# Kernel tuning notes

Hardware: AMD Instinct MI355X
Metric: run time of the kernel (lower is better)

The kernel has to match this reference:

```python
import jax, jax.numpy as jnp
import numpy as np

N, E, DIN, H, C, OUT = 50000, 400000, 128, 4, 64, 40
HC = H * C
NEG_SLOPE = 0.2
EPS = 1e-5


def setup_inputs() -> dict:
    keys = iter(jax.random.split(jax.random.key(0), 64))
    def rn(shape, s=1.0):
        return jax.random.normal(next(keys), shape, jnp.float32) * s
    w = 0.05  # small init scale keeps activations stable through 3 layers
    inp = {}
    inp["x"] = rn((N, DIN))
    inp["src"] = jax.random.randint(next(keys), (E,), 0, N, jnp.int32)
    inp["dst"] = jax.random.randint(next(keys), (E,), 0, N, jnp.int32)
    # conv0: 128 -> (H=4, C=64), concat -> 256
    inp["Wl0"] = rn((DIN, HC), w); inp["bl0"] = jnp.zeros((HC,), jnp.float32)
    inp["Wr0"] = rn((DIN, HC), w); inp["br0"] = jnp.zeros((HC,), jnp.float32)
    inp["att0"] = rn((H, C), w);   inp["bc0"] = jnp.zeros((HC,), jnp.float32)
    inp["Ws0"] = rn((DIN, HC), w); inp["bs0"] = jnp.zeros((HC,), jnp.float32)
    inp["g0"] = jnp.ones((HC,), jnp.float32); inp["be0"] = jnp.zeros((HC,), jnp.float32)
    # conv1: 256 -> (4, 64), concat -> 256
    inp["Wl1"] = rn((HC, HC), w); inp["bl1"] = jnp.zeros((HC,), jnp.float32)
    inp["Wr1"] = rn((HC, HC), w); inp["br1"] = jnp.zeros((HC,), jnp.float32)
    inp["att1"] = rn((H, C), w);  inp["bc1"] = jnp.zeros((HC,), jnp.float32)
    inp["Ws1"] = rn((HC, HC), w); inp["bs1"] = jnp.zeros((HC,), jnp.float32)
    inp["g1"] = jnp.ones((HC,), jnp.float32); inp["be1"] = jnp.zeros((HC,), jnp.float32)
    # conv2: 256 -> (4, 40), mean over heads -> 40
    inp["Wl2"] = rn((HC, H * OUT), w); inp["bl2"] = jnp.zeros((H * OUT,), jnp.float32)
    inp["Wr2"] = rn((HC, H * OUT), w); inp["br2"] = jnp.zeros((H * OUT,), jnp.float32)
    inp["att2"] = rn((H, OUT), w);     inp["bc2"] = jnp.zeros((OUT,), jnp.float32)
    inp["Ws2"] = rn((HC, OUT), w);     inp["bs2"] = jnp.zeros((OUT,), jnp.float32)
    return inp


def _gatv2_conv(x, s, d, Wl, bl, Wr, br, att, bc, concat):
    # PyG GATv2Conv: lin_l on source, lin_r on target; e = LeakyReLU(xl_j + xr_i);
    # logit = <e, att>; softmax over edges sharing the same target; msg = xl_j.
    n = x.shape[0]
    h, c = att.shape
    xl = (x @ Wl + bl).reshape(n, h, c)
    xr = (x @ Wr + br).reshape(n, h, c)
    e = jax.nn.leaky_relu(xl[s] + xr[d], NEG_SLOPE)           # [E, H, C]
    logit = jnp.einsum("ehc,hc->eh", e, att)                  # [E, H]
    m = jax.ops.segment_max(logit, d, num_segments=n)          # per-target max
    a = jnp.exp(logit - m[d])
    z = jax.ops.segment_sum(a, d, num_segments=n)
    alpha = a / z[d]                                           # segment softmax
    out = jax.ops.segment_sum(alpha[:, :, None] * xl[s], d, num_segments=n)  # [N,H,C]
    out = out.reshape(n, h * c) if concat else out.mean(axis=1)
    return out + bc


def _bn(x, g, b):
    mu = x.mean(axis=0)
    var = x.var(axis=0)
    return g * (x - mu) / jnp.sqrt(var + EPS) + b


def reference(x, src, dst,
              Wl0, bl0, Wr0, br0, att0, bc0, Ws0, bs0, g0, be0,
              Wl1, bl1, Wr1, br1, att1, bc1, Ws1, bs1, g1, be1,
              Wl2, bl2, Wr2, br2, att2, bc2, Ws2, bs2):
    n = x.shape[0]
    loops = jnp.arange(n, dtype=src.dtype)  # add_self_loops=True (PyG default)
    s = jnp.concatenate([src, loops])
    d = jnp.concatenate([dst, loops])
    x1 = _gatv2_conv(x, s, d, Wl0, bl0, Wr0, br0, att0, bc0, True) + (x @ Ws0 + bs0)
    x1 = jax.nn.relu(_bn(x1, g0, be0))
    h = _gatv2_conv(x1, s, d, Wl1, bl1, Wr1, br1, att1, bc1, True) + (x1 @ Ws1 + bs1)
    x2 = jax.nn.relu(_bn(h, g1, be1))
    out = _gatv2_conv(x2, s, d, Wl2, bl2, Wr2, br2, att2, bc2, False) + (x2 @ Ws2 + bs2)
    return (h, out)
```

## Files before the change

### kernel.cpp

```cpp
#include <hip/hip_runtime.h>
#include <hip/hip_bf16.h>
#include <cstdint>
#include <cstddef>

#define DIN 128
#define HC 256
#define OUTC 40
#define HOUT 160
#define NEG 0.2f
#define BNEPS 1e-5f

typedef float f32x4 __attribute__((ext_vector_type(4)));
typedef __bf16 bf16x8 __attribute__((ext_vector_type(8)));

struct __align__(8) bh4 { __hip_bfloat16 x, y, z, w; };

__device__ __forceinline__ float4 ld4(const float* p) { return *(const float4*)p; }

__device__ __forceinline__ float4 ldb4(const __hip_bfloat16* p) {
    bh4 v = *(const bh4*)p;
    return make_float4(__bfloat162float(v.x), __bfloat162float(v.y),
                       __bfloat162float(v.z), __bfloat162float(v.w));
}

__device__ __forceinline__ void load_lds16(const void* g, void* l) {
    __builtin_amdgcn_global_load_lds((const __attribute__((address_space(1))) void*)g,
                                     (__attribute__((address_space(3))) void*)l, 16, 0, 0);
}

__global__ __launch_bounds__(256)
void gemm_mfma(const __hip_bfloat16* __restrict__ A, const __hip_bfloat16* __restrict__ Wt,
               const float* __restrict__ biasc, __hip_bfloat16* __restrict__ Y,
               int M, int K, int Npad, int gx, int q, int r) {
    __shared__ __hip_bfloat16 smem[128 * 136];
    __hip_bfloat16* As = smem;
    __hip_bfloat16* Bs = smem + 128 * 32;
    const int tid = threadIdx.x;
    const int lane = tid & 63, wid = tid >> 6;
    const int wm = wid >> 1, wn = wid & 1;

    const int orig = blockIdx.x;
    const int xcd = orig & 7, pos = orig >> 3;
    const int wgid = (xcd < r ? xcd * (q + 1) : r * (q + 1) + (xcd - r) * q) + pos;
    const int bn = (wgid % gx) * 128, bm = (wgid / gx) * 128;

    const int srow = lane >> 2;
    const int sseg = (lane & 3) * 8;
    f32x4 acc[4][4] = {};

    for (int k0 = 0; k0 < K; k0 += 32) {
#pragma unroll
        for (int i = 0; i < 2; ++i) {
            int c = 2 * wid + i;
            int ar = bm + 16 * c + srow; if (ar >= M) ar = M - 1;
            load_lds16(A + (size_t)ar * K + k0 + sseg, (char*)As + c * 1024);
            int br = bn + 16 * c + srow;
            load_lds16(Wt + (size_t)br * K + k0 + sseg, (char*)Bs + c * 1024);
        }
        __syncthreads();
        const int rkb = (lane >> 4) * 8;
        bf16x8 af[4], bfr[4];
#pragma unroll
        for (int i = 0; i < 4; ++i) {
            af[i]  = *(const bf16x8*)(As + (wm * 64 + i * 16 + (lane & 15)) * 32 + rkb);
            bfr[i] = *(const bf16x8*)(Bs + (wn * 64 + i * 16 + (lane & 15)) * 32 + rkb);
        }
#pragma unroll
        for (int mi = 0; mi < 4; ++mi)
#pragma unroll
            for (int ni = 0; ni < 4; ++ni)
                acc[mi][ni] = __builtin_amdgcn_mfma_f32_16x16x32_bf16(af[mi], bfr[ni], acc[mi][ni], 0, 0, 0);
        __syncthreads();
    }
    const int cl = lane & 15, rg4 = (lane >> 4) * 4;
#pragma unroll
    for (int ni = 0; ni < 4; ++ni) {
        float bv = biasc[bn + wn * 64 + ni * 16 + cl];
#pragma unroll
        for (int mi = 0; mi < 4; ++mi)
#pragma unroll
            for (int rr = 0; rr < 4; ++rr)
                smem[(wm * 64 + mi * 16 + rg4 + rr) * 136 + wn * 64 + ni * 16 + cl] =
                    __float2bfloat16(acc[mi][ni][rr] + bv);
    }
    __syncthreads();
#pragma unroll
    for (int it = 0; it < 8; ++it) {
        int row = it * 16 + (tid >> 4);
        int gm = bm + row;
        if (gm < M) {
            float4 v = *(const float4*)((const char*)(smem + row * 136) + (tid & 15) * 16);
            *(float4*)(Y + (size_t)gm * Npad + bn + (tid & 15) * 8) = v;
        }
    }
}

__global__ void prep_w_kernel(const float* __restrict__ W0, const float* __restrict__ b0, int n0,
                              const float* __restrict__ W1, const float* __restrict__ b1, int n1,
                              const float* __restrict__ W2, const float* __restrict__ b2, int n2,
                              int K, int Npad, __hip_bfloat16* __restrict__ Wt,
                              float* __restrict__ bc) {
    int idx = blockIdx.x * 256 + threadIdx.x;
    if (idx >= Npad * K) return;
    int n = idx / K, k = idx % K;
    float v = 0.f, bb = 0.f;
    if (n < n0)                { v = W0[(size_t)k * n0 + n];             bb = b0[n]; }
    else if (n < n0 + n1)      { v = W1[(size_t)k * n1 + (n - n0)];      bb = b1[n - n0]; }
    else if (n < n0 + n1 + n2) { v = W2[(size_t)k * n2 + (n - n0 - n1)]; bb = b2[n - n0 - n1]; }
    Wt[(size_t)n * K + k] = __float2bfloat16(v);
    if (k == 0) bc[n] = bb;
}

__global__ void f2b_kernel(const float* __restrict__ X, __hip_bfloat16* __restrict__ Y, int n4) {
    int i = blockIdx.x * 256 + threadIdx.x;
    if (i >= n4) return;
    float4 v = ((const float4*)X)[i];
    bh4 o;
    o.x = __float2bfloat16(v.x); o.y = __float2bfloat16(v.y);
    o.z = __float2bfloat16(v.z); o.w = __float2bfloat16(v.w);
    ((bh4*)Y)[i] = o;
}

__global__ void hist_kernel(const int* __restrict__ dst, int* __restrict__ deg, int E) {
    int e = blockIdx.x * 256 + threadIdx.x;
    if (e < E) atomicAdd(&deg[dst[e]], 1);
}

__global__ __launch_bounds__(256)
void scan1_kernel(int* __restrict__ a, int* __restrict__ bsum, int n) {
    const int tid = threadIdx.x;
    const int i = blockIdx.x * 256 + tid;
    const int lane = tid & 63, w = tid >> 6;
    int v = (i < n) ? (a[i] + 1) : 0;
    int x = v;
#pragma unroll
    for (int s = 1; s < 64; s <<= 1) { int t = __shfl_up(x, s); if (lane >= s) x += t; }
    __shared__ int ws[4];
    if (lane == 63) ws[w] = x;
    __syncthreads();
    int bo = 0;
    if (w > 0) bo = ws[0];
    if (w > 1) bo += ws[1];
    if (w > 2) bo += ws[2];
    if (i <= n) a[i] = bo + x - v;
    if (tid == 255) bsum[blockIdx.x] = bo + x;
}

__global__ __launch_bounds__(256)
void scan2_kernel(int* __restrict__ bsum, int nb) {
    const int tid = threadIdx.x;
    const int lane = tid & 63, w = tid >> 6;
    int v = (tid < nb) ? bsum[tid] : 0;
    int x = v;
#pragma unroll
    for (int s = 1; s < 64; s <<= 1) { int t = __shfl_up(x, s); if (lane >= s) x += t; }
    __shared__ int ws[4];
    if (lane == 63) ws[w] = x;
    __syncthreads();
    int bo = 0;
    if (w > 0) bo = ws[0];
    if (w > 1) bo += ws[1];
    if (w > 2) bo += ws[2];
    if (tid < nb) bsum[tid] = bo + x - v;
}

__global__ void scan3_kernel(int* __restrict__ a, const int* __restrict__ bsum, int n) {
    int i = blockIdx.x * 256 + threadIdx.x;
    if (i <= n) a[i] += bsum[blockIdx.x];
}

__global__ void scatter_kernel(const int* __restrict__ src, const int* __restrict__ dst,
                               const int* __restrict__ off, int* __restrict__ cursor,
                               int* __restrict__ srcs, int E, int N) {
    int e = blockIdx.x * 256 + threadIdx.x;
    if (e >= E + N) return;
    int s, d;
    if (e < E) { s = src[e]; d = dst[e]; }
    else       { s = e - E;  d = e - E; }
    int p = atomicAdd(&cursor[d], 1);
    srcs[off[d] + p] = s;
}

__device__ __forceinline__ float edge_logit(const float4& xl, const float4& xr, const float4& av) {
    float ex = xl.x + xr.x; ex = ex > 0.f ? ex : NEG * ex;
    float ey = xl.y + xr.y; ey = ey > 0.f ? ey : NEG * ey;
    float ez = xl.z + xr.z; ez = ez > 0.f ? ez : NEG * ez;
    float ew = xl.w + xr.w; ew = ew > 0.f ? ew : NEG * ew;
    float p = ex * av.x + ey * av.y + ez * av.z + ew * av.w;
    p += __shfl_xor(p, 1);
    p += __shfl_xor(p, 2);
    p += __shfl_xor(p, 4);
    p += __shfl_xor(p, 8);
    return p;
}

__device__ __forceinline__ void ons_update(float p, const float4& xl, float& m, float& z,
                                           float& ax, float& ay, float& az, float& aw) {
    float mn = fmaxf(m, p);
    float sc = __expf(m - mn);
    float a  = __expf(p - mn);
    m = mn;
    z  = z  * sc + a;
    ax = ax * sc + a * xl.x;
    ay = ay * sc + a * xl.y;
    az = az * sc + a * xl.z;
    aw = aw * sc + a * xl.w;
}

__global__ __launch_bounds__(256)
void gat_conv_cat(const __hip_bfloat16* __restrict__ XL, const __hip_bfloat16* __restrict__ XR,
                  const __hip_bfloat16* __restrict__ SK, const float* __restrict__ att,
                  const float* __restrict__ bc,
                  const int* __restrict__ off, const int* __restrict__ srcs,
                  float* __restrict__ OUT, int N, int RS) {
    int n = blockIdx.x * 4 + (threadIdx.x >> 6);
    if (n >= N) return;
    int lane = threadIdx.x & 63;
    int c4 = lane << 2;
    const float4 xr = ldb4(XR + (size_t)n * RS + c4);
    const float4 av = ld4(att + c4);
    float m = -1e30f, z = 0.f;
    float ax = 0.f, ay = 0.f, az = 0.f, aw = 0.f;
    int j = off[n];
    const int e1 = off[n + 1];
    for (; j + 3 < e1; j += 4) {
        int s0 = srcs[j], s1 = srcs[j + 1], s2 = srcs[j + 2], s3 = srcs[j + 3];
        float4 xl0 = ldb4(XL + (size_t)s0 * RS + c4);
        float4 xl1 = ldb4(XL + (size_t)s1 * RS + c4);
        float4 xl2 = ldb4(XL + (size_t)s2 * RS + c4);
        float4 xl3 = ldb4(XL + (size_t)s3 * RS + c4);
        float p0 = edge_logit(xl0, xr, av);
        float p1 = edge_logit(xl1, xr, av);
        float p2 = edge_logit(xl2, xr, av);
        float p3 = edge_logit(xl3, xr, av);
        ons_update(p0, xl0, m, z, ax, ay, az, aw);
        ons_update(p1, xl1, m, z, ax, ay, az, aw);
        ons_update(p2, xl2, m, z, ax, ay, az, aw);
        ons_update(p3, xl3, m, z, ax, ay, az, aw);
    }
    for (; j < e1; ++j) {
        int s0 = srcs[j];
        float4 xl0 = ldb4(XL + (size_t)s0 * RS + c4);
        float p0 = edge_logit(xl0, xr, av);
        ons_update(p0, xl0, m, z, ax, ay, az, aw);
    }
    float inv = 1.f / z;
    float4 sk = ldb4(SK + (size_t)n * RS + c4);
    float4 bb = ld4(bc + c4);
    float4 r;
    r.x = ax * inv + bb.x + sk.x;
    r.y = ay * inv + bb.y + sk.y;
    r.z = az * inv + bb.z + sk.z;
    r.w = aw * inv + bb.w + sk.w;
    *(float4*)(OUT + (size_t)n * HC + c4) = r;
}

__global__ __launch_bounds__(256)
void gat_conv_mean(const __hip_bfloat16* __restrict__ XL, const __hip_bfloat16* __restrict__ XR,
                   const __hip_bfloat16* __restrict__ SK, const float* __restrict__ att,
                   const float* __restrict__ bc,
                   const int* __restrict__ off, const int* __restrict__ srcs,
                   float* __restrict__ OUT, int N, int RS) {
    int n = blockIdx.x * 4 + (threadIdx.x >> 6);
    if (n >= N) return;
    int lane = threadIdx.x & 63;
    int hd = lane >> 4, q = lane & 15;
    bool act = (q < 10);
    int base = hd * OUTC + (q << 2);
    float4 xr = make_float4(0.f, 0.f, 0.f, 0.f), av = xr;
    if (act) { xr = ldb4(XR + (size_t)n * RS + base); av = ld4(att + base); }
    float m = -1e30f, z = 0.f;
    float ax = 0.f, ay = 0.f, az = 0.f, aw = 0.f;
    int j = off[n];
    const int e1 = off[n + 1];
    const float4 zero = make_float4(0.f, 0.f, 0.f, 0.f);
    for (; j + 3 < e1; j += 4) {
        int s0 = srcs[j], s1 = srcs[j + 1], s2 = srcs[j + 2], s3 = srcs[j + 3];
        float4 xl0 = zero, xl1 = zero, xl2 = zero, xl3 = zero;
        if (act) {
            xl0 = ldb4(XL + (size_t)s0 * RS + base);
            xl1 = ldb4(XL + (size_t)s1 * RS + base);
            xl2 = ldb4(XL + (size_t)s2 * RS + base);
            xl3 = ldb4(XL + (size_t)s3 * RS + base);
        }
        float p0 = edge_logit(xl0, xr, av);
        float p1 = edge_logit(xl1, xr, av);
        float p2 = edge_logit(xl2, xr, av);
        float p3 = edge_logit(xl3, xr, av);
        ons_update(p0, xl0, m, z, ax, ay, az, aw);
        ons_update(p1, xl1, m, z, ax, ay, az, aw);
        ons_update(p2, xl2, m, z, ax, ay, az, aw);
        ons_update(p3, xl3, m, z, ax, ay, az, aw);
    }
    for (; j < e1; ++j) {
        int s0 = srcs[j];
        float4 xl0 = zero;
        if (act) xl0 = ldb4(XL + (size_t)s0 * RS + base);
        float p0 = edge_logit(xl0, xr, av);
        ons_update(p0, xl0, m, z, ax, ay, az, aw);
    }
    float inv = 1.f / z;
    float rx = ax * inv, ry = ay * inv, rz = az * inv, rw = aw * inv;
    rx += __shfl_xor(rx, 16); rx += __shfl_xor(rx, 32);
    ry += __shfl_xor(ry, 16); ry += __shfl_xor(ry, 32);
    rz += __shfl_xor(rz, 16); rz += __shfl_xor(rz, 32);
    rw += __shfl_xor(rw, 16); rw += __shfl_xor(rw, 32);
    if (lane < 10) {
        int o = q << 2;
        float4 sk = ldb4(SK + (size_t)n * RS + o);
        float4 r;
        r.x = rx * 0.25f + bc[o + 0] + sk.x;
        r.y = ry * 0.25f + bc[o + 1] + sk.y;
        r.z = rz * 0.25f + bc[o + 2] + sk.z;
        r.w = rw * 0.25f + bc[o + 3] + sk.w;
        *(float4*)(OUT + (size_t)n * OUTC + o) = r;
    }
}

__global__ __launch_bounds__(256)
void bn_stats_kernel(const float* __restrict__ X, float* __restrict__ sums,
                     float* __restrict__ sqs, int N) {
    int c = threadIdx.x;
    float s = 0.f, qq = 0.f;
    for (int n = blockIdx.x; n < N; n += gridDim.x) {
        float v = X[(size_t)n * HC + c];
        s += v; qq += v * v;
    }
    atomicAdd(&sums[c], s);
    atomicAdd(&sqs[c], qq);
}

__global__ __launch_bounds__(256)
void bn_finalize_kernel(const float* __restrict__ sums, const float* __restrict__ sqs,
                        const float* __restrict__ g, const float* __restrict__ be,
                        float* __restrict__ scale, float* __restrict__ shift, int N) {
    int c = threadIdx.x;
    float mean = sums[c] / (float)N;
    float var = sqs[c] / (float)N - mean * mean;
    float inv = rsqrtf(var + BNEPS);
    float sc = g[c] * inv;
    scale[c] = sc;
    shift[c] = be[c] - mean * sc;
}

__global__ __launch_bounds__(256)
void bn_apply_relu_kernel(const float* __restrict__ X, const float* __restrict__ sc,
                          const float* __restrict__ sh, __hip_bfloat16* __restrict__ Y, int n4) {
    for (int i = blockIdx.x * blockDim.x + threadIdx.x; i < n4; i += gridDim.x * blockDim.x) {
        int c4 = (i & 63) << 2;
        float4 v = ((const float4*)X)[i];
        float4 s = ld4(sc + c4);
        float4 h = ld4(sh + c4);
        bh4 r;
        r.x = __float2bfloat16(fmaxf(v.x * s.x + h.x, 0.f));
        r.y = __float2bfloat16(fmaxf(v.y * s.y + h.y, 0.f));
        r.z = __float2bfloat16(fmaxf(v.z * s.z + h.z, 0.f));
        r.w = __float2bfloat16(fmaxf(v.w * s.w + h.w, 0.f));
        ((bh4*)Y)[i] = r;
    }
}

extern "C" void kernel_launch(void* const* d_in, const int* in_sizes, int n_in,
                              void* d_out, int out_size, void* d_ws, size_t ws_size,
                              hipStream_t stream) {
    const int N = in_sizes[0] / DIN;
    const int E = in_sizes[1];
    const int Et = E + N;

    const float* x   = (const float*)d_in[0];
    const int* src   = (const int*)d_in[1];
    const int* dst   = (const int*)d_in[2];
    const float* Wl0 = (const float*)d_in[3];  const float* bl0 = (const float*)d_in[4];
    const float* Wr0 = (const float*)d_in[5];  const float* br0 = (const float*)d_in[6];
    const float* att0= (const float*)d_in[7];  const float* bc0 = (const float*)d_in[8];
    const float* Ws0 = (const float*)d_in[9];  const float* bs0 = (const float*)d_in[10];
    const float* g0  = (const float*)d_in[11]; const float* be0 = (const float*)d_in[12];
    const float* Wl1 = (const float*)d_in[13]; const float* bl1 = (const float*)d_in[14];
    const float* Wr1 = (const float*)d_in[15]; const float* br1 = (const float*)d_in[16];
    const float* att1= (const float*)d_in[17]; const float* bc1 = (const float*)d_in[18];
    const float* Ws1 = (const float*)d_in[19]; const float* bs1 = (const float*)d_in[20];
    const float* g1  = (const float*)d_in[21]; const float* be1 = (const float*)d_in[22];
    const float* Wl2 = (const float*)d_in[23]; const float* bl2 = (const float*)d_in[24];
    const float* Wr2 = (const float*)d_in[25]; const float* br2 = (const float*)d_in[26];
    const float* att2= (const float*)d_in[27]; const float* bc2 = (const float*)d_in[28];
    const float* Ws2 = (const float*)d_in[29]; const float* bs2 = (const float*)d_in[30];

    float* outh = (float*)d_out;
    float* outy = outh + (size_t)N * HC;

    __hip_bfloat16* Y  = (__hip_bfloat16*)d_ws;
    __hip_bfloat16* xb = Y + (size_t)N * 768;
    __hip_bfloat16* Wt = xb + (size_t)N * HC;
    float* bcc  = (float*)(Wt + 768 * 256);
    int* off    = (int*)(bcc + 768);
    int* cursor = off + (N + 1);
    int* srcs   = cursor + N;
    int* bsum   = srcs + Et;
    float* bn   = (float*)((((uintptr_t)(bsum + 256)) + 15) & ~(uintptr_t)15);

    const int nb_scan = (N + 1 + 255) / 256;
    hipMemsetAsync(off, 0, (size_t)(N + 1) * sizeof(int), stream);
    hipMemsetAsync(cursor, 0, (size_t)N * sizeof(int), stream);
    hist_kernel<<<(E + 255) / 256, 256, 0, stream>>>(dst, off, E);
    scan1_kernel<<<nb_scan, 256, 0, stream>>>(off, bsum, N);
    scan2_kernel<<<1, 256, 0, stream>>>(bsum, nb_scan);
    scan3_kernel<<<nb_scan, 256, 0, stream>>>(off, bsum, N);
    scatter_kernel<<<(Et + 255) / 256, 256, 0, stream>>>(src, dst, off, cursor, srcs, E, N);

    const int gmy = (N + 127) / 128;
    const int convGrid = (N + 3) / 4;
    const int nwgA = 6 * gmy, qA = nwgA / 8, rA = nwgA % 8;
    const int nwgC = 3 * gmy, qC = nwgC / 8, rC = nwgC % 8;

    f2b_kernel<<<(N * DIN / 4 + 255) / 256, 256, 0, stream>>>(x, xb, N * DIN / 4);
    prep_w_kernel<<<(768 * DIN + 255) / 256, 256, 0, stream>>>(
        Wl0, bl0, HC, Wr0, br0, HC, Ws0, bs0, HC, DIN, 768, Wt, bcc);
    gemm_mfma<<<nwgA, 256, 0, stream>>>(xb, Wt, bcc, Y, N, DIN, 768, 6, qA, rA);
    gat_conv_cat<<<convGrid, 256, 0, stream>>>(Y, Y + 256, Y + 512, att0, bc0, off, srcs,
                                               outh, N, 768);
    hipMemsetAsync(bn, 0, 512 * sizeof(float), stream);
    bn_stats_kernel<<<1024, 256, 0, stream>>>(outh, bn, bn + 256, N);
    bn_finalize_kernel<<<1, 256, 0, stream>>>(bn, bn + 256, g0, be0, bn + 512, bn + 768, N);
    bn_apply_relu_kernel<<<2048, 256, 0, stream>>>(outh, bn + 512, bn + 768, xb, N * (HC / 4));

    prep_w_kernel<<<(768 * HC + 255) / 256, 256, 0, stream>>>(
        Wl1, bl1, HC, Wr1, br1, HC, Ws1, bs1, HC, HC, 768, Wt, bcc);
    gemm_mfma<<<nwgA, 256, 0, stream>>>(xb, Wt, bcc, Y, N, HC, 768, 6, qA, rA);
    gat_conv_cat<<<convGrid, 256, 0, stream>>>(Y, Y + 256, Y + 512, att1, bc1, off, srcs,
                                               outh, N, 768);
    hipMemsetAsync(bn, 0, 512 * sizeof(float), stream);
    bn_stats_kernel<<<1024, 256, 0, stream>>>(outh, bn, bn + 256, N);
    bn_finalize_kernel<<<1, 256, 0, stream>>>(bn, bn + 256, g1, be1, bn + 512, bn + 768, N);
    bn_apply_relu_kernel<<<2048, 256, 0, stream>>>(outh, bn + 512, bn + 768, xb, N * (HC / 4));

    prep_w_kernel<<<(384 * HC + 255) / 256, 256, 0, stream>>>(
        Wl2, bl2, HOUT, Wr2, br2, HOUT, Ws2, bs2, OUTC, HC, 384, Wt, bcc);
    gemm_mfma<<<nwgC, 256, 0, stream>>>(xb, Wt, bcc, Y, N, HC, 384, 3, qC, rC);
    gat_conv_mean<<<convGrid, 256, 0, stream>>>(Y, Y + 160, Y + 320, att2, bc2, off, srcs,
                                                outy, N, 384);
}
```

Measured before the change: 448.9 us.

## Drop online-softmax max tracking and repack mean conv to half-wave per node

Replaces the online softmax, which rescales the running max on every edge, with a plain exp-sum accumulation. Logits are clamped at 50 to avoid overflow, so each edge no longer pays the extra exp and rescale multiplies. The head-mean conv now assigns 32 lanes per node (two nodes per wave), with each lane holding 5 channels (a float4 plus one scalar), so no lanes sit idle. The risk is reduced numerical robustness: large negative logits could underflow, and clamping changes results once logits exceed 50.

```diff
diff --git a/kernel.cpp b/kernel.cpp
--- a/kernel.cpp
+++ b/kernel.cpp
@@ -191,20 +191,7 @@
     p += __shfl_xor(p, 2);
     p += __shfl_xor(p, 4);
     p += __shfl_xor(p, 8);
-    return p;
-}
-
-__device__ __forceinline__ void ons_update(float p, const float4& xl, float& m, float& z,
-                                           float& ax, float& ay, float& az, float& aw) {
-    float mn = fmaxf(m, p);
-    float sc = __expf(m - mn);
-    float a  = __expf(p - mn);
-    m = mn;
-    z  = z  * sc + a;
-    ax = ax * sc + a * xl.x;
-    ay = ay * sc + a * xl.y;
-    az = az * sc + a * xl.z;
-    aw = aw * sc + a * xl.w;
+    return fminf(p, 50.f);
 }
 
 __global__ __launch_bounds__(256)
@@ -219,7 +206,7 @@
     int c4 = lane << 2;
     const float4 xr = ldb4(XR + (size_t)n * RS + c4);
     const float4 av = ld4(att + c4);
-    float m = -1e30f, z = 0.f;
+    float z = 0.f;
     float ax = 0.f, ay = 0.f, az = 0.f, aw = 0.f;
     int j = off[n];
     const int e1 = off[n + 1];
@@ -229,20 +216,20 @@
         float4 xl1 = ldb4(XL + (size_t)s1 * RS + c4);
         float4 xl2 = ldb4(XL + (size_t)s2 * RS + c4);
         float4 xl3 = ldb4(XL + (size_t)s3 * RS + c4);
-        float p0 = edge_logit(xl0, xr, av);
-        float p1 = edge_logit(xl1, xr, av);
-        float p2 = edge_logit(xl2, xr, av);
-        float p3 = edge_logit(xl3, xr, av);
-        ons_update(p0, xl0, m, z, ax, ay, az, aw);
-        ons_update(p1, xl1, m, z, ax, ay, az, aw);
-        ons_update(p2, xl2, m, z, ax, ay, az, aw);
-        ons_update(p3, xl3, m, z, ax, ay, az, aw);
+        float a0 = __expf(edge_logit(xl0, xr, av));
+        float a1 = __expf(edge_logit(xl1, xr, av));
+        float a2 = __expf(edge_logit(xl2, xr, av));
+        float a3 = __expf(edge_logit(xl3, xr, av));
+        z += a0; ax += a0 * xl0.x; ay += a0 * xl0.y; az += a0 * xl0.z; aw += a0 * xl0.w;
+        z += a1; ax += a1 * xl1.x; ay += a1 * xl1.y; az += a1 * xl1.z; aw += a1 * xl1.w;
+        z += a2; ax += a2 * xl2.x; ay += a2 * xl2.y; az += a2 * xl2.z; aw += a2 * xl2.w;
+        z += a3; ax += a3 * xl3.x; ay += a3 * xl3.y; az += a3 * xl3.z; aw += a3 * xl3.w;
     }
     for (; j < e1; ++j) {
         int s0 = srcs[j];
         float4 xl0 = ldb4(XL + (size_t)s0 * RS + c4);
-        float p0 = edge_logit(xl0, xr, av);
-        ons_update(p0, xl0, m, z, ax, ay, az, aw);
+        float a0 = __expf(edge_logit(xl0, xr, av));
+        z += a0; ax += a0 * xl0.x; ay += a0 * xl0.y; az += a0 * xl0.z; aw += a0 * xl0.w;
     }
     float inv = 1.f / z;
     float4 sk = ldb4(SK + (size_t)n * RS + c4);
@@ -255,65 +242,79 @@
     *(float4*)(OUT + (size_t)n * HC + c4) = r;
 }
 
+__device__ __forceinline__ void mean_edge(const __hip_bfloat16* __restrict__ XL, size_t srow,
+                                          int bm_ch, int bt_ch,
+                                          const float4& xr4, float xrt,
+                                          const float4& av4, float avt,
+                                          float& z, float& c0, float& c1, float& c2,
+                                          float& c3, float& c4) {
+    float4 x4 = ldb4(XL + srow + bm_ch);
+    float xt = __bfloat162float(XL[srow + bt_ch]);
+    float e0 = x4.x + xr4.x; e0 = e0 > 0.f ? e0 : NEG * e0;
+    float e1 = x4.y + xr4.y; e1 = e1 > 0.f ? e1 : NEG * e1;
+    float e2 = x4.z + xr4.z; e2 = e2 > 0.f ? e2 : NEG * e2;
+    float e3 = x4.w + xr4.w; e3 = e3 > 0.f ? e3 : NEG * e3;
+    float et = xt + xrt;     et = et > 0.f ? et : NEG * et;
+    float p = e0 * av4.x + e1 * av4.y + e2 * av4.z + e3 * av4.w + et * avt;
+    p += __shfl_xor(p, 1);
+    p += __shfl_xor(p, 2);
+    p += __shfl_xor(p, 4);
+    p = fminf(p, 50.f);
+    float a = __expf(p);
+    z += a;
+    c0 += a * x4.x; c1 += a * x4.y; c2 += a * x4.z; c3 += a * x4.w; c4 += a * xt;
+}
+
 __global__ __launch_bounds__(256)
 void gat_conv_mean(const __hip_bfloat16* __restrict__ XL, const __hip_bfloat16* __restrict__ XR,
                    const __hip_bfloat16* __restrict__ SK, const float* __restrict__ att,
                    const float* __restrict__ bc,
                    const int* __restrict__ off, const int* __restrict__ srcs,
                    float* __restrict__ OUT, int N, int RS) {
-    int n = blockIdx.x * 4 + (threadIdx.x >> 6);
+    const int lane = threadIdx.x & 63;
+    const int half = lane >> 5, sub = lane & 31;
+    const int n = blockIdx.x * 8 + (threadIdx.x >> 6) * 2 + half;
     if (n >= N) return;
-    int lane = threadIdx.x & 63;
-    int hd = lane >> 4, q = lane & 15;
-    bool act = (q < 10);
-    int base = hd * OUTC + (q << 2);
-    float4 xr = make_float4(0.f, 0.f, 0.f, 0.f), av = xr;
-    if (act) { xr = ldb4(XR + (size_t)n * RS + base); av = ld4(att + base); }
-    float m = -1e30f, z = 0.f;
-    float ax = 0.f, ay = 0.f, az = 0.f, aw = 0.f;
+    const int hd = sub >> 3, q = sub & 7;
+    const int bm_ch = hd * OUTC + q * 4;
+    const int bt_ch = hd * OUTC + 32 + q;
+    const size_t nrow = (size_t)n * RS;
+    const float4 xr4 = ldb4(XR + nrow + bm_ch);
+    const float xrt = __bfloat162float(XR[nrow + bt_ch]);
+    const float4 av4 = ld4(att + bm_ch);
+    const float avt = att[bt_ch];
+    float z = 0.f, c0 = 0.f, c1 = 0.f, c2 = 0.f, c3 = 0.f, c4 = 0.f;
     int j = off[n];
     const int e1 = off[n + 1];
-    const float4 zero = make_float4(0.f, 0.f, 0.f, 0.f);
     for (; j + 3 < e1; j += 4) {
-        int s0 = srcs[j], s1 = srcs[j + 1], s2 = srcs[j + 2], s3 = srcs[j + 3];
-        float4 xl0 = zero, xl1 = zero, xl2 = zero, xl3 = zero;
-        if (act) {
-            xl0 = ldb4(XL + (size_t)s0 * RS + base);
-            xl1 = ldb4(XL + (size_t)s1 * RS + base);
-            xl2 = ldb4(XL + (size_t)s2 * RS + base);
-            xl3 = ldb4(XL + (size_t)s3 * RS + base);
-        }
-        float p0 = edge_logit(xl0, xr, av);
-        float p1 = edge_logit(xl1, xr, av);
-        float p2 = edge_logit(xl2, xr, av);
-        float p3 = edge_logit(xl3, xr, av);
-        ons_update(p0, xl0, m, z, ax, ay, az, aw);
-        ons_update(p1, xl1, m, z, ax, ay, az, aw);
-        ons_update(p2, xl2, m, z, ax, ay, az, aw);
-        ons_update(p3, xl3, m, z, ax, ay, az, aw);
-    }
-    for (; j < e1; ++j) {
-        int s0 = srcs[j];
-        float4 xl0 = zero;
-        if (act) xl0 = ldb4(XL + (size_t)s0 * RS + base);
-        float p0 = edge_logit(xl0, xr, av);
-        ons_update(p0, xl0, m, z, ax, ay, az, aw);
-    }
+        size_t r0 = (size_t)srcs[j] * RS,     r1 = (size_t)srcs[j + 1] * RS;
+        size_t r2 = (size_t)srcs[j + 2] * RS, r3 = (size_t)srcs[j + 3] * RS;
+        mean_edge(XL, r0, bm_ch, bt_ch, xr4, xrt, av4, avt, z, c0, c1, c2, c3, c4);
+        mean_edge(XL, r1, bm_ch, bt_ch, xr4, xrt, av4, avt, z, c0, c1, c2, c3, c4);
+        mean_edge(XL, r2, bm_ch, bt_ch, xr4, xrt, av4, avt, z, c0, c1, c2, c3, c4);
+        mean_edge(XL, r3, bm_ch, bt_ch, xr4, xrt, av4, avt, z, c0, c1, c2, c3, c4);
+    }
+    for (; j < e1; ++j)
+        mean_edge(XL, (size_t)srcs[j] * RS, bm_ch, bt_ch, xr4, xrt, av4, avt, z, c0, c1, c2, c3, c4);
+
     float inv = 1.f / z;
-    float rx = ax * inv, ry = ay * inv, rz = az * inv, rw = aw * inv;
-    rx += __shfl_xor(rx, 16); rx += __shfl_xor(rx, 32);
-    ry += __shfl_xor(ry, 16); ry += __shfl_xor(ry, 32);
-    rz += __shfl_xor(rz, 16); rz += __shfl_xor(rz, 32);
-    rw += __shfl_xor(rw, 16); rw += __shfl_xor(rw, 32);
-    if (lane < 10) {
+    float r0 = c0 * inv, r1 = c1 * inv, r2 = c2 * inv, r3 = c3 * inv, r4 = c4 * inv;
+    r0 += __shfl_xor(r0, 8); r0 += __shfl_xor(r0, 16);
+    r1 += __shfl_xor(r1, 8); r1 += __shfl_xor(r1, 16);
+    r2 += __shfl_xor(r2, 8); r2 += __shfl_xor(r2, 16);
+    r3 += __shfl_xor(r3, 8); r3 += __shfl_xor(r3, 16);
+    r4 += __shfl_xor(r4, 8); r4 += __shfl_xor(r4, 16);
+    if (hd == 0) {
         int o = q << 2;
-        float4 sk = ldb4(SK + (size_t)n * RS + o);
-        float4 r;
-        r.x = rx * 0.25f + bc[o + 0] + sk.x;
-        r.y = ry * 0.25f + bc[o + 1] + sk.y;
-        r.z = rz * 0.25f + bc[o + 2] + sk.z;
-        r.w = rw * 0.25f + bc[o + 3] + sk.w;
-        *(float4*)(OUT + (size_t)n * OUTC + o) = r;
+        float4 sk4 = ldb4(SK + nrow + o);
+        float skt = __bfloat162float(SK[nrow + 32 + q]);
+        float4 rv;
+        rv.x = r0 * 0.25f + bc[o + 0] + sk4.x;
+        rv.y = r1 * 0.25f + bc[o + 1] + sk4.y;
+        rv.z = r2 * 0.25f + bc[o + 2] + sk4.z;
+        rv.w = r3 * 0.25f + bc[o + 3] + sk4.w;
+        *(float4*)(OUT + (size_t)n * OUTC + o) = rv;
+        OUT[(size_t)n * OUTC + 32 + q] = r4 * 0.25f + bc[32 + q] + skt;
     }
 }
 
@@ -409,6 +410,7 @@
 
     const int gmy = (N + 127) / 128;
     const int convGrid = (N + 3) / 4;
+    const int meanGrid = (N + 7) / 8;
     const int nwgA = 6 * gmy, qA = nwgA / 8, rA = nwgA % 8;
     const int nwgC = 3 * gmy, qC = nwgC / 8, rC = nwgC % 8;
 
@@ -436,6 +438,6 @@
     prep_w_kernel<<<(384 * HC + 255) / 256, 256, 0, stream>>>(
         Wl2, bl2, HOUT, Wr2, br2, HOUT, Ws2, bs2, OUTC, HC, 384, Wt, bcc);
     gemm_mfma<<<nwgC, 256, 0, stream>>>(xb, Wt, bcc, Y, N, HC, 384, 3, qC, rC);
-    gat_conv_mean<<<convGrid, 256, 0, stream>>>(Y, Y + 160, Y + 320, att2, bc2, off, srcs,
+    gat_conv_mean<<<meanGrid, 256, 0, stream>>>(Y, Y + 160, Y + 320, att2, bc2, off, srcs,
                                                 outy, N, 384);
 }
```

Result: faster. 427.7 us (-4.7%).
